# Performance work log

Hardware: AMD Instinct MI355X
Metric: run time of the kernel (lower is better)

Reference implementation:

```python
import jax, jax.numpy as jnp
import numpy as np

ATTENTION_HEAD = 16
EXPANSION_LENGTH = 300
TEXT_EMBEDDING_DIM = 768
LN_EPS = 1e-3  # keras LayerNormalization default epsilon


def setup_inputs() -> dict:
    key = jax.random.key(0)
    ks = jax.random.split(key, 8)
    B, L, D = 8, 2048, TEXT_EMBEDDING_DIM
    H = ATTENTION_HEAD
    E = EXPANSION_LENGTH
    dh = D // H
    glorot = lambda k, shape, fan_in, fan_out: jax.random.uniform(
        k, shape, jnp.float32,
        -jnp.sqrt(6.0 / (fan_in + fan_out)), jnp.sqrt(6.0 / (fan_in + fan_out)))
    return {
        "q": jax.random.normal(ks[0], (B, 1, L, D), jnp.float32),
        "k": jax.random.normal(ks[1], (B, 1, L, D), jnp.float32),
        "v": jax.random.normal(ks[2], (B, 1, L, D), jnp.float32),
        "Wq": glorot(ks[3], (D, D), D, D),
        "bq": jnp.zeros((D,), jnp.float32),
        "Wv": glorot(ks[4], (D, D), D, D),
        "bv": jnp.zeros((D,), jnp.float32),
        "memory": glorot(ks[5], (E, H, dh), E, dh),
        "gamma": jnp.ones((D,), jnp.float32),
        "beta": jnp.zeros((D,), jnp.float32),
    }


def reference(q, k, v, Wq, bq, Wv, bv, memory, gamma, beta):
    B, _, L, D = q.shape
    H = ATTENTION_HEAD
    dh = D // H
    # Dense projections (v is unused by the original module)
    Q_ = q @ Wq + bq                      # (B,1,L,D)
    V_ = k @ Wv + bv                      # (B,1,L,D)
    Q = Q_.reshape(B, L, H, dh)
    V = V_.reshape(B, L, H, dh)
    # memory-query scores, ReLU instead of softmax
    eij = jax.nn.relu(jnp.einsum('ehd,blhd->belh', memory, Q))  # (B,E,L,H)
    out1 = jnp.einsum('belh,blhd->behd', eij, V)                # (B,E,H,dh)
    out2 = jnp.einsum('behd,belh->blhd', out1, eij)             # (B,L,H,dh)
    x = out2.reshape(B, 1, L, D)
    mean = jnp.mean(x, axis=-1, keepdims=True)
    var = jnp.var(x, axis=-1, keepdims=True)
    return (x - mean) * jax.lax.rsqrt(var + LN_EPS) * gamma + beta
```

## Files before the change

kernel.cpp:

```cpp
#include <hip/hip_runtime.h>
#include <hip/hip_bf16.h>
#include <stdint.h>

#define B_   8
#define L_   2048
#define D_   768
#define H_   16
#define DH   48
#define E_   300
#define EP   320
#define KP   64
#define ACH  4
#define N1T  (128 * DH * EP)

typedef __bf16 bf16;
typedef __bf16 bf16x8 __attribute__((ext_vector_type(8)));
typedef __bf16 bf16x4 __attribute__((ext_vector_type(4)));
typedef float  f32x4  __attribute__((ext_vector_type(4)));

typedef const __attribute__((address_space(1))) uint32_t guint;
typedef __attribute__((address_space(3))) uint32_t luint;

__device__ __forceinline__ f32x4 mfma16(bf16x8 a, bf16x8 b, f32x4 c) {
  return __builtin_amdgcn_mfma_f32_16x16x32_bf16(a, b, c, 0, 0, 0);
}

__global__ __launch_bounds__(256) void k_wt(const float* __restrict__ Wq,
                                            const float* __restrict__ Wv,
                                            bf16* __restrict__ WqT,
                                            bf16* __restrict__ WvT) {
  int idx = blockIdx.x * 256 + threadIdx.x;
  int n = idx / D_, k = idx % D_;
  const float* W = blockIdx.y ? Wv : Wq;
  bf16* WT = blockIdx.y ? WvT : WqT;
  WT[n * D_ + k] = (bf16)W[k * D_ + n];
}

__global__ __launch_bounds__(256) void k_mem(const float* __restrict__ M,
                                             bf16* __restrict__ MP) {
  int idx = blockIdx.x * 256 + threadIdx.x;
  int h = idx / (EP * KP);
  int r = idx % (EP * KP);
  int e = r / KP, d = r % KP;
  float v = (e < E_ && d < DH) ? M[(e * H_ + h) * DH + d] : 0.f;
  MP[idx] = (bf16)v;
}

__global__ __launch_bounds__(256) void k_gemm(
    const float* __restrict__ A0, const float* __restrict__ A1,
    const bf16* __restrict__ WT0, const bf16* __restrict__ WT1,
    const float* __restrict__ b0, const float* __restrict__ b1,
    bf16* __restrict__ outQ, bf16* __restrict__ outVT) {
  __shared__ bf16 As[128 * 40];
  __shared__ bf16 Bs[128 * 32];
  const int tid = threadIdx.x, lane = tid & 63, w = tid >> 6;
  const int wr = w >> 1, wc = w & 1;
  const int lr = lane & 15, lq = lane >> 4;
  const int n0 = blockIdx.x * 128, m0 = blockIdx.y * 128;
  const int mode = blockIdx.z;
  const float* A = mode ? A1 : A0;
  const bf16* WT = mode ? WT1 : WT0;
  const float* bias = mode ? b1 : b0;

  f32x4 acc[4][4] = {};

  for (int k0 = 0; k0 < D_; k0 += 32) {
    __syncthreads();
#pragma unroll
    for (int t = 0; t < 2; ++t) {
      int idx = tid + t * 256;
      int row = idx >> 2, c8 = idx & 3;
      const float* src = A + (size_t)(m0 + row) * D_ + k0 + c8 * 8;
      float4 f0 = *(const float4*)src;
      float4 f1 = *(const float4*)(src + 4);
      bf16x8 v;
      v[0] = (bf16)f0.x; v[1] = (bf16)f0.y; v[2] = (bf16)f0.z; v[3] = (bf16)f0.w;
      v[4] = (bf16)f1.x; v[5] = (bf16)f1.y; v[6] = (bf16)f1.z; v[7] = (bf16)f1.w;
      *(bf16x8*)&As[row * 40 + c8 * 8] = v;
    }
#pragma unroll
    for (int t = 0; t < 2; ++t) {
      const bf16* src = WT + (size_t)(n0 + t * 64 + (tid >> 2)) * D_ + k0 + (tid & 3) * 8;
      __builtin_amdgcn_global_load_lds((guint*)src, (luint*)&Bs[t * 2048 + w * 512], 16, 0, 0);
    }
    __syncthreads();
    bf16x8 af[4], bfr[4];
#pragma unroll
    for (int mi = 0; mi < 4; ++mi)
      af[mi] = *(const bf16x8*)&As[(wr * 64 + mi * 16 + lr) * 40 + lq * 8];
#pragma unroll
    for (int ni = 0; ni < 4; ++ni)
      bfr[ni] = *(const bf16x8*)&Bs[(wc * 64 + ni * 16 + lr) * 32 + lq * 8];
#pragma unroll
    for (int mi = 0; mi < 4; ++mi)
#pragma unroll
      for (int ni = 0; ni < 4; ++ni)
        acc[mi][ni] = mfma16(af[mi], bfr[ni], acc[mi][ni]);
  }

  float bs[4];
#pragma unroll
  for (int ni = 0; ni < 4; ++ni) bs[ni] = bias[n0 + wc * 64 + ni * 16 + lr];

  if (mode == 0) {
#pragma unroll
    for (int mi = 0; mi < 4; ++mi)
#pragma unroll
      for (int ni = 0; ni < 4; ++ni) {
        int m = m0 + wr * 64 + mi * 16 + lq * 4;
        int n = n0 + wc * 64 + ni * 16 + lr;
#pragma unroll
        for (int r = 0; r < 4; ++r)
          outQ[(size_t)(m + r) * D_ + n] = (bf16)(acc[mi][ni][r] + bs[ni]);
      }
  } else {
#pragma unroll
    for (int mi = 0; mi < 4; ++mi)
#pragma unroll
      for (int ni = 0; ni < 4; ++ni) {
        int mb = m0 + wr * 64 + mi * 16 + lq * 4;
        int n = n0 + wc * 64 + ni * 16 + lr;
        int bhd = (mb >> 11) * H_ + n / DH;
        int d = n % DH;
        int l = mb & (L_ - 1);
        bf16x4 v;
#pragma unroll
        for (int r = 0; r < 4; ++r) v[r] = (bf16)(acc[mi][ni][r] + bs[ni]);
        *(bf16x4*)&outVT[((size_t)bhd * DH + d) * L_ + l] = v;
      }
  }
}

__global__ __launch_bounds__(256) void k_phaseA(
    const bf16* __restrict__ Qb, const bf16* __restrict__ VT,
    const bf16* __restrict__ MP, float* __restrict__ O1P) {
  __shared__ bf16 Qs[2][32 * 88];
  __shared__ bf16 Vs[2][48 * 40];
  __shared__ bf16 Ss[EP * 40];
  const int tid = threadIdx.x, lane = tid & 63, w = tid >> 6;
  const int lr = lane & 15, lq = lane >> 4;
  const int bh = blockIdx.y, b = bh >> 4, h = bh & 15;
  const int lbase = blockIdx.x * (L_ / ACH);

  bf16x8 mf[5][2];
#pragma unroll
  for (int mi = 0; mi < 5; ++mi)
#pragma unroll
    for (int kh = 0; kh < 2; ++kh)
      mf[mi][kh] = *(const bf16x8*)&MP[(size_t)(h * EP + w * 80 + mi * 16 + lr) * KP + kh * 32 + lq * 8];

  if (tid < 128) {
    int buf = tid >> 6, t = tid & 63;
    uint4 z = {0, 0, 0, 0};
    *(uint4*)&Qs[buf][(t >> 1) * 88 + 48 + (t & 1) * 8] = z;
  }

  auto loadQ = [&](int idx, int l0) {
    return *(const bf16x8*)&Qb[(size_t)(b * L_ + l0 + idx / 6) * D_ + h * DH + (idx % 6) * 8];
  };
  auto loadV = [&](int j, int l0) {
    return *(const bf16x8*)&VT[((size_t)bh * DH + (j >> 2)) * L_ + l0 + (j & 3) * 8];
  };

  bf16x8 rA, rB;
  {
    int l0 = lbase;
    rA = (tid < 192) ? loadQ(tid, l0) : loadV(tid - 192, l0);
    if (tid < 128) rB = loadV(tid + 64, l0);
  }

  f32x4 acc[5][3] = {};

  for (int it = 0; it < L_ / ACH / 32; ++it) {
    const int cur = it & 1;
    if (tid < 192) *(bf16x8*)&Qs[cur][(tid / 6) * 88 + (tid % 6) * 8] = rA;
    else           *(bf16x8*)&Vs[cur][((tid - 192) >> 2) * 40 + ((tid - 192) & 3) * 8] = rA;
    if (tid < 128) *(bf16x8*)&Vs[cur][((tid + 64) >> 2) * 40 + ((tid + 64) & 3) * 8] = rB;
    __syncthreads();
    if (it + 1 < L_ / ACH / 32) {
      int l0 = lbase + (it + 1) * 32;
      rA = (tid < 192) ? loadQ(tid, l0) : loadV(tid - 192, l0);
      if (tid < 128) rB = loadV(tid + 64, l0);
    }
    bf16x8 qf[2][2];
#pragma unroll
    for (int ni = 0; ni < 2; ++ni)
#pragma unroll
      for (int kh = 0; kh < 2; ++kh)
        qf[ni][kh] = *(const bf16x8*)&Qs[cur][(ni * 16 + lr) * 88 + kh * 32 + lq * 8];
#pragma unroll
    for (int mi = 0; mi < 5; ++mi)
#pragma unroll
      for (int ni = 0; ni < 2; ++ni) {
        f32x4 s = {0.f, 0.f, 0.f, 0.f};
        s = mfma16(mf[mi][0], qf[ni][0], s);
        s = mfma16(mf[mi][1], qf[ni][1], s);
#pragma unroll
        for (int r = 0; r < 4; ++r)
          Ss[(w * 80 + mi * 16 + lq * 4 + r) * 40 + ni * 16 + lr] =
              (bf16)(s[r] > 0.f ? s[r] : 0.f);
      }
    bf16x8 sf[5], vf[3];
#pragma unroll
    for (int mi = 0; mi < 5; ++mi)
      sf[mi] = *(const bf16x8*)&Ss[(w * 80 + mi * 16 + lr) * 40 + lq * 8];
#pragma unroll
    for (int ni = 0; ni < 3; ++ni)
      vf[ni] = *(const bf16x8*)&Vs[cur][(ni * 16 + lr) * 40 + lq * 8];
#pragma unroll
    for (int mi = 0; mi < 5; ++mi)
#pragma unroll
      for (int ni = 0; ni < 3; ++ni)
        acc[mi][ni] = mfma16(sf[mi], vf[ni], acc[mi][ni]);
  }
  float* dst = O1P + (size_t)(blockIdx.x * 128 + bh) * DH * EP;
#pragma unroll
  for (int mi = 0; mi < 5; ++mi)
#pragma unroll
    for (int ni = 0; ni < 3; ++ni) {
      int e = w * 80 + mi * 16 + lq * 4;
      int d = ni * 16 + lr;
#pragma unroll
      for (int r = 0; r < 4; ++r)
        dst[(size_t)d * EP + e + r] = acc[mi][ni][r];
    }
}

__global__ __launch_bounds__(256) void k_red(const float* __restrict__ O1P,
                                             bf16* __restrict__ O1T) {
  int idx = blockIdx.x * 256 + threadIdx.x;
  if (idx >= N1T) return;
  float s = O1P[idx];
#pragma unroll
  for (int c = 1; c < ACH; ++c) s += O1P[(size_t)c * N1T + idx];
  O1T[idx] = (bf16)s;
}

__global__ __launch_bounds__(256, 4) void k_phaseB(
    const bf16* __restrict__ Qb, const bf16* __restrict__ MP,
    const bf16* __restrict__ O1T, bf16* __restrict__ X) {
  __shared__ bf16 Qs[64 * 88];
  __shared__ bf16 STs[64 * 76];
  __shared__ bf16 O1s[2][48 * 76];
  const int tid = threadIdx.x, lane = tid & 63, w = tid >> 6;
  const int lr = lane & 15, lq = lane >> 4;
  const int bh = blockIdx.y, b = bh >> 4, h = bh & 15;
  const int l0 = blockIdx.x * 64;

  bf16x8 mfB[5][2];
#pragma unroll
  for (int c = 0; c < 5; ++c)
#pragma unroll
    for (int kh = 0; kh < 2; ++kh)
      mfB[c][kh] = *(const bf16x8*)&MP[(size_t)(h * EP + c * 64 + w * 16 + lr) * KP + kh * 32 + lq * 8];

  for (int idx = tid; idx < 512; idx += 256) {
    if (idx < 384) {
      int row = idx / 6, c = idx % 6;
      *(bf16x8*)&Qs[row * 88 + c * 8] =
          *(const bf16x8*)&Qb[(size_t)(b * L_ + l0 + row) * D_ + h * DH + c * 8];
    } else {
      int j = idx - 384;
      uint4 z = {0, 0, 0, 0};
      *(uint4*)&Qs[(j >> 1) * 88 + 48 + (j & 1) * 8] = z;
    }
  }
  for (int idx = tid; idx < 384; idx += 256)
    *(bf16x8*)&O1s[0][(idx >> 3) * 76 + (idx & 7) * 8] =
        *(const bf16x8*)&O1T[((size_t)bh * DH + (idx >> 3)) * EP + (idx & 7) * 8];
  __syncthreads();

  f32x4 acc[3] = {};
#pragma unroll
  for (int c = 0; c < 5; ++c) {
    bf16x8 r0, r1;
    if (c < 4) {
      r0 = *(const bf16x8*)&O1T[((size_t)bh * DH + (tid >> 3)) * EP + (c + 1) * 64 + (tid & 7) * 8];
      if (tid < 128) {
        int i2 = tid + 256;
        r1 = *(const bf16x8*)&O1T[((size_t)bh * DH + (i2 >> 3)) * EP + (c + 1) * 64 + (i2 & 7) * 8];
      }
    }
#pragma unroll
    for (int mi = 0; mi < 4; ++mi) {
      bf16x8 qa0 = *(const bf16x8*)&Qs[(mi * 16 + lr) * 88 + lq * 8];
      bf16x8 qa1 = *(const bf16x8*)&Qs[(mi * 16 + lr) * 88 + 32 + lq * 8];
      f32x4 s = {0.f, 0.f, 0.f, 0.f};
      s = mfma16(qa0, mfB[c][0], s);
      s = mfma16(qa1, mfB[c][1], s);
#pragma unroll
      for (int r = 0; r < 4; ++r)
        STs[(mi * 16 + lq * 4 + r) * 76 + w * 16 + lr] =
            (bf16)(s[r] > 0.f ? s[r] : 0.f);
    }
    __syncthreads();
#pragma unroll
    for (int ks = 0; ks < 2; ++ks) {
      bf16x8 sf = *(const bf16x8*)&STs[(w * 16 + lr) * 76 + ks * 32 + lq * 8];
#pragma unroll
      for (int ni = 0; ni < 3; ++ni) {
        bf16x8 of = *(const bf16x8*)&O1s[c & 1][(ni * 16 + lr) * 76 + ks * 32 + lq * 8];
        acc[ni] = mfma16(sf, of, acc[ni]);
      }
    }
    if (c < 4) {
      *(bf16x8*)&O1s[(c + 1) & 1][(tid >> 3) * 76 + (tid & 7) * 8] = r0;
      if (tid < 128) {
        int i2 = tid + 256;
        *(bf16x8*)&O1s[(c + 1) & 1][(i2 >> 3) * 76 + (i2 & 7) * 8] = r1;
      }
    }
    __syncthreads();
  }
#pragma unroll
  for (int ni = 0; ni < 3; ++ni)
#pragma unroll
    for (int r = 0; r < 4; ++r)
      X[(size_t)(b * L_ + l0 + w * 16 + lq * 4 + r) * D_ + h * DH + ni * 16 + lr] =
          (bf16)acc[ni][r];
}

__global__ __launch_bounds__(256) void k_ln(
    const bf16* __restrict__ X, const float* __restrict__ gamma,
    const float* __restrict__ beta, float* __restrict__ out) {
  const int row = blockIdx.x, tid = threadIdx.x;
  const bf16* x = X + (size_t)row * D_;
  float v0 = (float)x[tid], v1 = (float)x[tid + 256], v2 = (float)x[tid + 512];
  float s = v0 + v1 + v2;
  float q = v0 * v0 + v1 * v1 + v2 * v2;
#pragma unroll
  for (int off = 32; off > 0; off >>= 1) {
    s += __shfl_xor(s, off);
    q += __shfl_xor(q, off);
  }
  __shared__ float rs[4], rq[4];
  if ((tid & 63) == 0) { rs[tid >> 6] = s; rq[tid >> 6] = q; }
  __syncthreads();
  float S = rs[0] + rs[1] + rs[2] + rs[3];
  float Q2 = rq[0] + rq[1] + rq[2] + rq[3];
  float mean = S * (1.f / 768.f);
  float var = Q2 * (1.f / 768.f) - mean * mean;
  float inv = rsqrtf(var + 1e-3f);
  float* o = out + (size_t)row * D_;
  o[tid] = (v0 - mean) * inv * gamma[tid] + beta[tid];
  o[tid + 256] = (v1 - mean) * inv * gamma[tid + 256] + beta[tid + 256];
  o[tid + 512] = (v2 - mean) * inv * gamma[tid + 512] + beta[tid + 512];
}

extern "C" void kernel_launch(void* const* d_in, const int* in_sizes, int n_in,
                              void* d_out, int out_size, void* d_ws, size_t ws_size,
                              hipStream_t stream) {
  (void)in_sizes; (void)n_in; (void)out_size; (void)ws_size;
  const float* q_in = (const float*)d_in[0];
  const float* k_in = (const float*)d_in[1];
  const float* Wq   = (const float*)d_in[3];
  const float* bq   = (const float*)d_in[4];
  const float* Wv   = (const float*)d_in[5];
  const float* bv   = (const float*)d_in[6];
  const float* mem  = (const float*)d_in[7];
  const float* gam  = (const float*)d_in[8];
  const float* bet  = (const float*)d_in[9];
  float* out = (float*)d_out;

  char* ws = (char*)d_ws;
  size_t off = 0;
  auto alloc = [&](size_t bytes) {
    char* p = ws + off;
    off += (bytes + 255) & ~(size_t)255;
    return p;
  };
  bf16*  WqT = (bf16*)alloc((size_t)D_ * D_ * 2);
  bf16*  WvT = (bf16*)alloc((size_t)D_ * D_ * 2);
  bf16*  MP  = (bf16*)alloc((size_t)H_ * EP * KP * 2);
  bf16*  Qb  = (bf16*)alloc((size_t)B_ * L_ * D_ * 2);
  bf16*  VT  = (bf16*)alloc((size_t)B_ * H_ * DH * L_ * 2);
  bf16*  O1T = (bf16*)alloc((size_t)N1T * 2);
  char*  big = alloc((size_t)ACH * N1T * 4);
  float* O1P = (float*)big;
  bf16*  Xb  = (bf16*)big;

  k_wt<<<dim3((D_ * D_) / 256, 2), 256, 0, stream>>>(Wq, Wv, WqT, WvT);
  k_mem<<<(H_ * EP * KP) / 256, 256, 0, stream>>>(mem, MP);
  k_gemm<<<dim3(6, 128, 2), 256, 0, stream>>>(q_in, k_in, WqT, WvT, bq, bv, Qb, VT);
  k_phaseA<<<dim3(ACH, B_ * H_), 256, 0, stream>>>(Qb, VT, MP, O1P);
  k_red<<<(N1T + 255) / 256, 256, 0, stream>>>(O1P, O1T);
  k_phaseB<<<dim3(L_ / 64, B_ * H_), 256, 0, stream>>>(Qb, MP, O1T, Xb);
  k_ln<<<B_ * L_, 256, 0, stream>>>(Xb, gam, bet, out);
}
```

Measured before the change: 210.5 us.

## Pre-cast inputs to bf16, widen GEMM tiles, and use wave-per-row LayerNorm

A separate kernel now converts q and k to bf16 so the projection GEMM can load A tiles straight into LDS with global_load_lds instead of converting fp32 in registers. The GEMM tile grows to 128x256 with a swizzled 1D block index intended to improve L2 reuse, at the cost of more accumulator registers. LayerNorm now handles one row per wave with vectorized loads and no shared-memory reduction. The cast adds an extra full read and write of both inputs, and the bf16 copies share workspace with later buffers.

```diff
diff --git a/kernel.cpp b/kernel.cpp
--- a/kernel.cpp
+++ b/kernel.cpp
@@ -25,6 +25,23 @@
   return __builtin_amdgcn_mfma_f32_16x16x32_bf16(a, b, c, 0, 0, 0);
 }
 
+__global__ __launch_bounds__(256) void k_cast(const float* __restrict__ q,
+                                              const float* __restrict__ k,
+                                              bf16* __restrict__ qc,
+                                              bf16* __restrict__ kc) {
+  const float* src = blockIdx.y ? k : q;
+  bf16* dst = blockIdx.y ? kc : qc;
+  const int n8 = B_ * L_ * D_ / 8;
+  for (int i = blockIdx.x * 256 + threadIdx.x; i < n8; i += gridDim.x * 256) {
+    float4 f0 = *(const float4*)(src + (size_t)i * 8);
+    float4 f1 = *(const float4*)(src + (size_t)i * 8 + 4);
+    bf16x8 v;
+    v[0] = (bf16)f0.x; v[1] = (bf16)f0.y; v[2] = (bf16)f0.z; v[3] = (bf16)f0.w;
+    v[4] = (bf16)f1.x; v[5] = (bf16)f1.y; v[6] = (bf16)f1.z; v[7] = (bf16)f1.w;
+    *(bf16x8*)(dst + (size_t)i * 8) = v;
+  }
+}
+
 __global__ __launch_bounds__(256) void k_wt(const float* __restrict__ Wq,
                                             const float* __restrict__ Wv,
                                             bf16* __restrict__ WqT,
@@ -47,68 +64,65 @@
 }
 
 __global__ __launch_bounds__(256) void k_gemm(
-    const float* __restrict__ A0, const float* __restrict__ A1,
+    const bf16* __restrict__ A0, const bf16* __restrict__ A1,
     const bf16* __restrict__ WT0, const bf16* __restrict__ WT1,
     const float* __restrict__ b0, const float* __restrict__ b1,
     bf16* __restrict__ outQ, bf16* __restrict__ outVT) {
-  __shared__ bf16 As[128 * 40];
-  __shared__ bf16 Bs[128 * 32];
+  __shared__ bf16 As[128 * 32];
+  __shared__ bf16 Bs[256 * 32];
   const int tid = threadIdx.x, lane = tid & 63, w = tid >> 6;
   const int wr = w >> 1, wc = w & 1;
   const int lr = lane & 15, lq = lane >> 4;
-  const int n0 = blockIdx.x * 128, m0 = blockIdx.y * 128;
-  const int mode = blockIdx.z;
-  const float* A = mode ? A1 : A0;
+  const int bid = blockIdx.x;
+  const int j = (bid & 7) * 48 + (bid >> 3);
+  const int n0 = (j % 3) * 256, m0 = (j / 3) * 128;
+  const int mode = blockIdx.y;
+  const bf16* A = mode ? A1 : A0;
   const bf16* WT = mode ? WT1 : WT0;
   const float* bias = mode ? b1 : b0;
 
-  f32x4 acc[4][4] = {};
+  f32x4 acc[4][8] = {};
 
   for (int k0 = 0; k0 < D_; k0 += 32) {
     __syncthreads();
 #pragma unroll
     for (int t = 0; t < 2; ++t) {
       int idx = tid + t * 256;
-      int row = idx >> 2, c8 = idx & 3;
-      const float* src = A + (size_t)(m0 + row) * D_ + k0 + c8 * 8;
-      float4 f0 = *(const float4*)src;
-      float4 f1 = *(const float4*)(src + 4);
-      bf16x8 v;
-      v[0] = (bf16)f0.x; v[1] = (bf16)f0.y; v[2] = (bf16)f0.z; v[3] = (bf16)f0.w;
-      v[4] = (bf16)f1.x; v[5] = (bf16)f1.y; v[6] = (bf16)f1.z; v[7] = (bf16)f1.w;
-      *(bf16x8*)&As[row * 40 + c8 * 8] = v;
-    }
-#pragma unroll
-    for (int t = 0; t < 2; ++t) {
-      const bf16* src = WT + (size_t)(n0 + t * 64 + (tid >> 2)) * D_ + k0 + (tid & 3) * 8;
+      const bf16* src = A + (size_t)(m0 + (idx >> 2)) * D_ + k0 + (idx & 3) * 8;
+      __builtin_amdgcn_global_load_lds((guint*)src, (luint*)&As[t * 2048 + w * 512], 16, 0, 0);
+    }
+#pragma unroll
+    for (int t = 0; t < 4; ++t) {
+      int idx = tid + t * 256;
+      const bf16* src = WT + (size_t)(n0 + (idx >> 2)) * D_ + k0 + (idx & 3) * 8;
       __builtin_amdgcn_global_load_lds((guint*)src, (luint*)&Bs[t * 2048 + w * 512], 16, 0, 0);
     }
     __syncthreads();
-    bf16x8 af[4], bfr[4];
+    bf16x8 af[4], bfr[8];
 #pragma unroll
     for (int mi = 0; mi < 4; ++mi)
-      af[mi] = *(const bf16x8*)&As[(wr * 64 + mi * 16 + lr) * 40 + lq * 8];
-#pragma unroll
-    for (int ni = 0; ni < 4; ++ni)
-      bfr[ni] = *(const bf16x8*)&Bs[(wc * 64 + ni * 16 + lr) * 32 + lq * 8];
+      af[mi] = *(const bf16x8*)&As[(wr * 64 + mi * 16 + lr) * 32 + lq * 8];
+#pragma unroll
+    for (int ni = 0; ni < 8; ++ni)
+      bfr[ni] = *(const bf16x8*)&Bs[(wc * 128 + ni * 16 + lr) * 32 + lq * 8];
 #pragma unroll
     for (int mi = 0; mi < 4; ++mi)
 #pragma unroll
-      for (int ni = 0; ni < 4; ++ni)
+      for (int ni = 0; ni < 8; ++ni)
         acc[mi][ni] = mfma16(af[mi], bfr[ni], acc[mi][ni]);
   }
 
-  float bs[4];
-#pragma unroll
-  for (int ni = 0; ni < 4; ++ni) bs[ni] = bias[n0 + wc * 64 + ni * 16 + lr];
+  float bs[8];
+#pragma unroll
+  for (int ni = 0; ni < 8; ++ni) bs[ni] = bias[n0 + wc * 128 + ni * 16 + lr];
 
   if (mode == 0) {
 #pragma unroll
     for (int mi = 0; mi < 4; ++mi)
 #pragma unroll
-      for (int ni = 0; ni < 4; ++ni) {
+      for (int ni = 0; ni < 8; ++ni) {
         int m = m0 + wr * 64 + mi * 16 + lq * 4;
-        int n = n0 + wc * 64 + ni * 16 + lr;
+        int n = n0 + wc * 128 + ni * 16 + lr;
 #pragma unroll
         for (int r = 0; r < 4; ++r)
           outQ[(size_t)(m + r) * D_ + n] = (bf16)(acc[mi][ni][r] + bs[ni]);
@@ -117,9 +131,9 @@
 #pragma unroll
     for (int mi = 0; mi < 4; ++mi)
 #pragma unroll
-      for (int ni = 0; ni < 4; ++ni) {
+      for (int ni = 0; ni < 8; ++ni) {
         int mb = m0 + wr * 64 + mi * 16 + lq * 4;
-        int n = n0 + wc * 64 + ni * 16 + lr;
+        int n = n0 + wc * 128 + ni * 16 + lr;
         int bhd = (mb >> 11) * H_ + n / DH;
         int d = n % DH;
         int l = mb & (L_ - 1);
@@ -323,28 +337,39 @@
 __global__ __launch_bounds__(256) void k_ln(
     const bf16* __restrict__ X, const float* __restrict__ gamma,
     const float* __restrict__ beta, float* __restrict__ out) {
-  const int row = blockIdx.x, tid = threadIdx.x;
+  const int lane = threadIdx.x & 63;
+  const int row = blockIdx.x * 4 + (threadIdx.x >> 6);
   const bf16* x = X + (size_t)row * D_;
-  float v0 = (float)x[tid], v1 = (float)x[tid + 256], v2 = (float)x[tid + 512];
-  float s = v0 + v1 + v2;
-  float q = v0 * v0 + v1 * v1 + v2 * v2;
+  float v[12];
+#pragma unroll
+  for (int c = 0; c < 3; ++c) {
+    bf16x4 ch = *(const bf16x4*)(x + lane * 12 + c * 4);
+#pragma unroll
+    for (int j = 0; j < 4; ++j) v[c * 4 + j] = (float)ch[j];
+  }
+  float s = 0.f, q = 0.f;
+#pragma unroll
+  for (int j = 0; j < 12; ++j) { s += v[j]; q += v[j] * v[j]; }
 #pragma unroll
   for (int off = 32; off > 0; off >>= 1) {
     s += __shfl_xor(s, off);
     q += __shfl_xor(q, off);
   }
-  __shared__ float rs[4], rq[4];
-  if ((tid & 63) == 0) { rs[tid >> 6] = s; rq[tid >> 6] = q; }
-  __syncthreads();
-  float S = rs[0] + rs[1] + rs[2] + rs[3];
-  float Q2 = rq[0] + rq[1] + rq[2] + rq[3];
-  float mean = S * (1.f / 768.f);
-  float var = Q2 * (1.f / 768.f) - mean * mean;
+  float mean = s * (1.f / 768.f);
+  float var = q * (1.f / 768.f) - mean * mean;
   float inv = rsqrtf(var + 1e-3f);
   float* o = out + (size_t)row * D_;
-  o[tid] = (v0 - mean) * inv * gamma[tid] + beta[tid];
-  o[tid + 256] = (v1 - mean) * inv * gamma[tid + 256] + beta[tid + 256];
-  o[tid + 512] = (v2 - mean) * inv * gamma[tid + 512] + beta[tid + 512];
+#pragma unroll
+  for (int c = 0; c < 3; ++c) {
+    float4 g = *(const float4*)(gamma + lane * 12 + c * 4);
+    float4 bt = *(const float4*)(beta + lane * 12 + c * 4);
+    float4 r;
+    r.x = (v[c * 4 + 0] - mean) * inv * g.x + bt.x;
+    r.y = (v[c * 4 + 1] - mean) * inv * g.y + bt.y;
+    r.z = (v[c * 4 + 2] - mean) * inv * g.z + bt.z;
+    r.w = (v[c * 4 + 3] - mean) * inv * g.w + bt.w;
+    *(float4*)(o + lane * 12 + c * 4) = r;
+  }
 }
 
 extern "C" void kernel_launch(void* const* d_in, const int* in_sizes, int n_in,
@@ -375,15 +400,21 @@
   bf16*  Qb  = (bf16*)alloc((size_t)B_ * L_ * D_ * 2);
   bf16*  VT  = (bf16*)alloc((size_t)B_ * H_ * DH * L_ * 2);
   bf16*  O1T = (bf16*)alloc((size_t)N1T * 2);
-  char*  big = alloc((size_t)ACH * N1T * 4);
+  const size_t castHalf = ((size_t)B_ * L_ * D_ * 2 + 256) & ~(size_t)255;
+  const size_t castBytes = 2 * castHalf;
+  const size_t o1pBytes  = (size_t)ACH * N1T * 4;
+  char*  big = alloc(castBytes > o1pBytes ? castBytes : o1pBytes);
+  bf16*  qc  = (bf16*)big;
+  bf16*  kc  = (bf16*)(big + castHalf);
   float* O1P = (float*)big;
   bf16*  Xb  = (bf16*)big;
 
+  k_cast<<<dim3(2048, 2), 256, 0, stream>>>(q_in, k_in, qc, kc);
   k_wt<<<dim3((D_ * D_) / 256, 2), 256, 0, stream>>>(Wq, Wv, WqT, WvT);
   k_mem<<<(H_ * EP * KP) / 256, 256, 0, stream>>>(mem, MP);
-  k_gemm<<<dim3(6, 128, 2), 256, 0, stream>>>(q_in, k_in, WqT, WvT, bq, bv, Qb, VT);
+  k_gemm<<<dim3(384, 2), 256, 0, stream>>>(qc, kc, WqT, WvT, bq, bv, Qb, VT);
   k_phaseA<<<dim3(ACH, B_ * H_), 256, 0, stream>>>(Qb, VT, MP, O1P);
   k_red<<<(N1T + 255) / 256, 256, 0, stream>>>(O1P, O1T);
   k_phaseB<<<dim3(L_ / 64, B_ * H_), 256, 0, stream>>>(Qb, MP, O1T, Xb);
-  k_ln<<<B_ * L_, 256, 0, stream>>>(Xb, gam, bet, out);
-}
+  k_ln<<<(B_ * L_) / 4, 256, 0, stream>>>(Xb, gam, bet, out);
+}
```

Result: slower. 221.2 us (+5.1%).
